# Kernel optimization log

Measured on AMD Instinct MI355X. Metric: run time of the kernel, lower is better.

The kernel has to match this reference:

```python
import jax, jax.numpy as jnp
import numpy as np

N, D_IN, D_OUT, E = 100000, 64, 64, 800000
C_IN, C_OUT = 1.0, 1.0
MAX_NORM = 1e6   # manifold.max_norm clamp used by PseudoHypAgg
EPS = 1e-15
BALL_EPS = 4e-3  # Poincare-ball projection margin (fp32)


def _artanh(x):
    return jnp.arctanh(jnp.clip(x, -1 + 1e-7, 1 - 1e-7))


def _proj(x, c):
    # project onto the open Poincare ball of curvature c
    sqrt_c = jnp.sqrt(c)
    norm = jnp.clip(jnp.linalg.norm(x, axis=-1, keepdims=True), EPS)
    maxn = (1.0 - BALL_EPS) / sqrt_c
    return jnp.where(norm > maxn, x / norm * maxn, x)


def _expmap0(u, c):
    sqrt_c = jnp.sqrt(c)
    n = jnp.clip(jnp.linalg.norm(u, axis=-1, keepdims=True), EPS)
    return jnp.tanh(sqrt_c * n) * u / (sqrt_c * n)


def _logmap0(p, c):
    sqrt_c = jnp.sqrt(c)
    n = jnp.clip(jnp.linalg.norm(p, axis=-1, keepdims=True), EPS)
    return _artanh(sqrt_c * n) * p / (sqrt_c * n)


def _mobius_add(x, y, c):
    x2 = jnp.sum(x * x, -1, keepdims=True)
    y2 = jnp.sum(y * y, -1, keepdims=True)
    xy = jnp.sum(x * y, -1, keepdims=True)
    num = (1 + 2 * c * xy + c * y2) * x + (1 - c * x2) * y
    den = 1 + 2 * c * xy + c * c * x2 * y2
    return num / jnp.clip(den, EPS)


def _mobius_matvec(M, x, c):
    sqrt_c = jnp.sqrt(c)
    x_norm = jnp.clip(jnp.linalg.norm(x, axis=-1, keepdims=True), EPS)
    mx = x @ M.T  # [N, D_OUT]
    mx_norm = jnp.clip(jnp.linalg.norm(mx, axis=-1, keepdims=True), EPS)
    res = jnp.tanh(mx_norm / x_norm * _artanh(sqrt_c * x_norm)) * mx / (mx_norm * sqrt_c)
    zero = jnp.all(mx == 0, axis=-1, keepdims=True)
    return jnp.where(zero, jnp.zeros_like(res), res)


def setup_inputs() -> dict:
    key = jax.random.key(0)
    k1, k2, k3, k4, k5, k6 = jax.random.split(key, 6)
    # node features: small-norm points inside the unit ball
    x = _proj(0.05 * jax.random.normal(k1, (N, D_IN), jnp.float32), C_IN)
    W = jax.random.normal(k2, (D_OUT, D_IN), jnp.float32) / np.float32(np.sqrt(D_IN))
    b = 0.01 * jax.random.normal(k3, (D_OUT,), jnp.float32)
    edge_row = jax.random.randint(k4, (E,), 0, N, jnp.int32)
    edge_col = jax.random.randint(k5, (E,), 0, N, jnp.int32)
    edge_val = jax.random.uniform(k6, (E,), jnp.float32) / 16.0  # ~normalized adj weights
    return {"x": x, "W": W, "b": b, "edge_row": edge_row,
            "edge_col": edge_col, "edge_val": edge_val}


def reference(x, W, b, edge_row, edge_col, edge_val):
    # --- PseudoHypLinear (eval mode: dropout inactive) ---
    mv = _mobius_matvec(W, x, C_IN)
    res = _proj(mv, C_IN)
    hyp_b = _proj(_expmap0(b[None, :], C_IN), C_IN)  # proj_tan0 is identity on the ball
    h = _proj(_mobius_add(res, hyp_b, C_IN), C_IN)
    # --- PseudoHypAgg (use_att=False): spmm in tangent space at origin ---
    x_t = _logmap0(h, C_IN)                              # [N, D_OUT]
    msg = edge_val[:, None] * x_t[edge_col]              # [E, D_OUT]
    support_t = jax.ops.segment_sum(msg, edge_row, num_segments=N)
    support_t = jnp.minimum(support_t, MAX_NORM)         # clamp(max=manifold.max_norm)
    h = _proj(_expmap0(support_t, C_IN), C_IN)           # proj_tan0 identity
    # --- PseudoHypAct: act in tangent at origin (c_in), re-embed with c_out ---
    xt = jax.nn.relu(_logmap0(h, C_IN))
    return _proj(_expmap0(xt, C_OUT), C_OUT)
```

## Files before the change

### kernel.cpp

```cpp
#include <hip/hip_runtime.h>
#include <hip/hip_fp16.h>
#include <math.h>

#define DD 64
#define BK 128
#define BCAP 2048
#define NBKT_MAX 800
#define CHUNK 8192
constexpr float FEPS = 1e-15f;
constexpr float MAXN = 1.0f - 4e-3f;

__device__ __forceinline__ float wsum(float v) {
    v += __shfl_xor(v, 32);
    v += __shfl_xor(v, 16);
    v += __shfl_xor(v, 8);
    v += __shfl_xor(v, 4);
    v += __shfl_xor(v, 2);
    v += __shfl_xor(v, 1);
    return v;
}

__device__ __forceinline__ int wave_incl_scan(int v) {
    int lane = threadIdx.x & 63;
    #pragma unroll
    for (int d = 1; d < 64; d <<= 1) {
        int t = __shfl_up(v, d);
        if (lane >= d) v += t;
    }
    return v;
}

__device__ __forceinline__ float artanh_c(float x) {
    x = fminf(fmaxf(x, -1.f + 1e-7f), 1.f - 1e-7f);
    return 0.5f * logf((1.f + x) / (1.f - x));
}

struct SmemLin {
    float tile[DD * 65];
    float red0[8][DD];
    float red1[8][DD];
    float hb[66];
};
struct SmemBin {
    int lcnt[NBKT_MAX];
    int goff[NBKT_MAX];
};

__global__ __launch_bounds__(512) void kfused(
    const float* __restrict__ x, const float* __restrict__ W,
    const float* __restrict__ bvec, __half* __restrict__ xth,
    const int* __restrict__ erow, const int* __restrict__ ecol,
    const float* __restrict__ eval_, int* __restrict__ gcnt,
    int2* __restrict__ binned, int nbkt, int n_edges, int n_nodes, int nbL) {
    __shared__ union { SmemLin lin; SmemBin bin; } sm;
    const int t = threadIdx.x;

    if ((int)blockIdx.x >= nbL) {
        const int eb = ((int)blockIdx.x - nbL) * CHUNK;
        for (int i = t; i < nbkt; i += 512) sm.bin.lcnt[i] = 0;
        __syncthreads();
        int rk[16];
        #pragma unroll
        for (int i = 0; i < 16; ++i) {
            int e = eb + i * 512 + t;
            rk[i] = -1;
            if (e < n_edges) {
                int r = erow[e];
                int bkt = r >> 7;
                int rank = atomicAdd(&sm.bin.lcnt[bkt], 1);
                rk[i] = (bkt << 20) | ((r & (BK - 1)) << 13) | rank;
            }
        }
        __syncthreads();
        for (int i = t; i < nbkt; i += 512) {
            int c = sm.bin.lcnt[i];
            if (c > 0) sm.bin.goff[i] = atomicAdd(&gcnt[i], c);
        }
        __syncthreads();
        #pragma unroll
        for (int i = 0; i < 16; ++i) {
            int e = eb + i * 512 + t;
            if (e >= n_edges) continue;
            int bkt = rk[i] >> 20, lr = (rk[i] >> 13) & 127, rank = rk[i] & 8191;
            int pos = sm.bin.goff[bkt] + rank;
            if (pos < BCAP)
                binned[(size_t)bkt * BCAP + pos] =
                    make_int2((lr << 17) | ecol[e], __float_as_int(eval_[e]));
        }
        return;
    }

    const int lane = t & 63;
    const int w = t >> 6;
    const int n0 = blockIdx.x * DD;

    #pragma unroll
    for (int rep = 0; rep < 2; ++rep) {
        int i = rep * 512 + t;
        int nd = i >> 4, q = i & 15;
        int node = n0 + nd;
        const float4* src = reinterpret_cast<const float4*>(
            x + (size_t)(node < n_nodes ? node : 0) * DD);
        float4 v = src[q];
        float* d = &sm.lin.tile[nd * 65 + q * 4];
        d[0] = v.x; d[1] = v.y; d[2] = v.z; d[3] = v.w;
    }
    if (t < 64) {
        float bv = bvec[t];
        float n2 = wsum(bv * bv);
        float n = fmaxf(sqrtf(n2), FEPS);
        float th = tanhf(n);
        float p = th * (bv / n);
        float pn = th * (sqrtf(n2) / n);
        float pn_c = fmaxf(pn, FEPS);
        if (pn_c > MAXN) p *= MAXN / pn_c;
        sm.lin.hb[t] = p;
        float p2 = wsum(p * p);
        if (t == 0) sm.lin.hb[DD] = p2;
    }
    __syncthreads();

    const int jbase = __builtin_amdgcn_readfirstlane(w) * 8;
    float mx[8] = {0.f, 0.f, 0.f, 0.f, 0.f, 0.f, 0.f, 0.f};
    float xn2 = 0.f;
    #pragma unroll
    for (int kk = 0; kk < 4; ++kk) {
        float xv[16];
        #pragma unroll
        for (int ki = 0; ki < 16; ++ki)
            xv[ki] = sm.lin.tile[lane * 65 + kk * 16 + ki];
        #pragma unroll
        for (int ki = 0; ki < 16; ++ki)
            xn2 = fmaf(xv[ki], xv[ki], xn2);
        #pragma unroll
        for (int jj = 0; jj < 8; ++jj) {
            const float* Wr = W + (jbase + jj) * DD + kk * 16;
            float a = mx[jj];
            #pragma unroll
            for (int ki = 0; ki < 16; ++ki) a = fmaf(Wr[ki], xv[ki], a);
            mx[jj] = a;
        }
    }
    float mx2p = 0.f, mxhp = 0.f;
    #pragma unroll
    for (int jj = 0; jj < 8; ++jj) {
        mx2p = fmaf(mx[jj], mx[jj], mx2p);
        mxhp = fmaf(mx[jj], sm.lin.hb[jbase + jj], mxhp);
    }
    sm.lin.red0[w][lane] = mx2p;
    sm.lin.red1[w][lane] = mxhp;
    __syncthreads();
    float mx2 = 0.f, mxh = 0.f;
    #pragma unroll
    for (int ww = 0; ww < 8; ++ww) {
        mx2 += sm.lin.red0[ww][lane];
        mxh += sm.lin.red1[ww][lane];
    }

    float xn = fmaxf(sqrtf(xn2), FEPS);
    float mxn = fmaxf(sqrtf(mx2), FEPS);
    float th = tanhf((mxn / xn) * artanh_c(xn));
    float sres = (mx2 == 0.f) ? 0.f : th / mxn;
    float rn = (mx2 == 0.f) ? 0.f : th * (sqrtf(mx2) / mxn);
    float rn_c = fmaxf(rn, FEPS);
    float s1 = (rn_c > MAXN) ? sres * (MAXN / rn_c) : sres;
    float x2r = s1 * s1 * mx2;
    float xy = s1 * mxh;
    float y2 = sm.lin.hb[DD];
    float ca = 1.f + 2.f * xy + y2;
    float cb = 1.f - x2r;
    float rden = 1.f / fmaxf(1.f + 2.f * xy + x2r * y2, FEPS);
    float al = ca * s1 * rden;
    float be = cb * rden;
    float h2 = al * al * mx2 + 2.f * al * be * mxh + be * be * y2;
    float hn = fmaxf(sqrtf(h2), FEPS);
    float sh = 1.f;
    if (hn > MAXN) { sh = MAXN / hn; hn = MAXN; }
    float su = sh * (artanh_c(hn) / hn);
    float A = su * al, B = su * be;

    #pragma unroll
    for (int jj = 0; jj < 8; ++jj)
        sm.lin.tile[lane * 65 + jbase + jj] =
            fmaf(A, mx[jj], B * sm.lin.hb[jbase + jj]);
    __syncthreads();

    uint2* dst = reinterpret_cast<uint2*>(xth + (size_t)n0 * DD);
    #pragma unroll
    for (int rep = 0; rep < 2; ++rep) {
        int i = rep * 512 + t;
        int nd = i >> 4, q = i & 15;
        if (n0 + nd < n_nodes) {
            const float* s = &sm.lin.tile[nd * 65 + q * 4];
            __half2 h0 = __floats2half2_rn(s[0], s[1]);
            __half2 h1 = __floats2half2_rn(s[2], s[3]);
            uint2 o;
            o.x = *reinterpret_cast<unsigned int*>(&h0);
            o.y = *reinterpret_cast<unsigned int*>(&h1);
            dst[i] = o;
        }
    }
}

__device__ __forceinline__ void agg_epilogue(
    float4 acc, int row, int fl, float* __restrict__ out) {
    float4 s;
    s.x = fminf(acc.x, 1e6f); s.y = fminf(acc.y, 1e6f);
    s.z = fminf(acc.z, 1e6f); s.w = fminf(acc.w, 1e6f);
    float4 rs;
    rs.x = fmaxf(s.x, 0.f); rs.y = fmaxf(s.y, 0.f);
    rs.z = fmaxf(s.z, 0.f); rs.w = fmaxf(s.w, 0.f);
    float n2p = s.x * s.x + s.y * s.y + s.z * s.z + s.w * s.w;
    float sp2p = rs.x * rs.x + rs.y * rs.y + rs.z * rs.z + rs.w * rs.w;
    #pragma unroll
    for (int m = 1; m < 16; m <<= 1) {
        n2p += __shfl_xor(n2p, m);
        sp2p += __shfl_xor(sp2p, m);
    }
    float n = fmaxf(sqrtf(n2p), FEPS);
    float th = tanhf(n);
    float c1 = th / n;
    float pn = th * (sqrtf(n2p) / n);
    float pn_c = fmaxf(pn, FEPS);
    if (pn_c > MAXN) { c1 *= MAXN / pn_c; pn_c = MAXN; }
    float k1 = (artanh_c(pn_c) / pn_c) * c1;
    float u2 = k1 * k1 * sp2p;
    float un = fmaxf(sqrtf(u2), FEPS);
    float t2 = tanhf(un);
    float k2 = (t2 / un) * k1;
    float on = t2 * (sqrtf(u2) / un);
    float on_c = fmaxf(on, FEPS);
    if (on_c > MAXN) k2 *= MAXN / on_c;
    float4 o;
    o.x = k2 * rs.x; o.y = k2 * rs.y; o.z = k2 * rs.z; o.w = k2 * rs.w;
    reinterpret_cast<float4*>(out)[(size_t)row * 16 + fl] = o;
}

__global__ __launch_bounds__(512) void kagg2(
    const int* __restrict__ gcnt, const int2* __restrict__ binned,
    const __half* __restrict__ xth, float* __restrict__ out, int n_nodes) {
    __shared__ int hist[BK], offs[BK], cur[BK];
    __shared__ int2 srt[BCAP];
    const int t = threadIdx.x;
    const int b = blockIdx.x;
    for (int i = t; i < BK; i += 512) hist[i] = 0;
    __syncthreads();
    const int nrec = min(gcnt[b], BCAP);
    const int2* rec = binned + (size_t)b * BCAP;
    int2 rc[BCAP / 512];
    #pragma unroll
    for (int i = 0; i < BCAP / 512; ++i) {
        int j = i * 512 + t;
        if (j < nrec) {
            rc[i] = rec[j];
            atomicAdd(&hist[rc[i].x >> 17], 1);
        }
    }
    __syncthreads();
    if (t < 64) {
        int v = hist[t];
        int s = wave_incl_scan(v);
        offs[t] = s - v;
    }
    __syncthreads();
    if (t < 64) {
        int c = offs[63] + hist[63];
        int v = hist[64 + t];
        int s = wave_incl_scan(v);
        offs[64 + t] = c + s - v;
    }
    __syncthreads();
    for (int i = t; i < BK; i += 512) cur[i] = offs[i];
    __syncthreads();
    #pragma unroll
    for (int i = 0; i < BCAP / 512; ++i) {
        int j = i * 512 + t;
        if (j < nrec) {
            int lr = rc[i].x >> 17;
            int p = atomicAdd(&cur[lr], 1);
            srt[p] = make_int2(rc[i].x & 0x1FFFF, rc[i].y);
        }
    }
    __syncthreads();

    const int g = t >> 4, fl = t & 15;
    #pragma unroll
    for (int it = 0; it < BK / 32; ++it) {
        int lr = it * 32 + g;
        int row = b * BK + lr;
        if (row >= n_nodes) continue;
        int beg = offs[lr], end = beg + hist[lr];
        float4 acc = make_float4(0.f, 0.f, 0.f, 0.f);
        int j = beg;
        for (; j + 3 < end; j += 4) {
            int2 e0 = srt[j], e1 = srt[j + 1], e2 = srt[j + 2], e3 = srt[j + 3];
            float2 r0 = *reinterpret_cast<const float2*>(xth + (size_t)e0.x * DD + fl * 4);
            float2 r1 = *reinterpret_cast<const float2*>(xth + (size_t)e1.x * DD + fl * 4);
            float2 r2 = *reinterpret_cast<const float2*>(xth + (size_t)e2.x * DD + fl * 4);
            float2 r3 = *reinterpret_cast<const float2*>(xth + (size_t)e3.x * DD + fl * 4);
            float w0 = __int_as_float(e0.y), w1 = __int_as_float(e1.y);
            float w2 = __int_as_float(e2.y), w3 = __int_as_float(e3.y);
            float2 a0 = __half22float2(*reinterpret_cast<__half2*>(&r0.x));
            float2 a1 = __half22float2(*reinterpret_cast<__half2*>(&r0.y));
            float2 b0 = __half22float2(*reinterpret_cast<__half2*>(&r1.x));
            float2 b1 = __half22float2(*reinterpret_cast<__half2*>(&r1.y));
            float2 c0 = __half22float2(*reinterpret_cast<__half2*>(&r2.x));
            float2 c1 = __half22float2(*reinterpret_cast<__half2*>(&r2.y));
            float2 d0 = __half22float2(*reinterpret_cast<__half2*>(&r3.x));
            float2 d1 = __half22float2(*reinterpret_cast<__half2*>(&r3.y));
            acc.x = fmaf(w0, a0.x, acc.x); acc.y = fmaf(w0, a0.y, acc.y);
            acc.z = fmaf(w0, a1.x, acc.z); acc.w = fmaf(w0, a1.y, acc.w);
            acc.x = fmaf(w1, b0.x, acc.x); acc.y = fmaf(w1, b0.y, acc.y);
            acc.z = fmaf(w1, b1.x, acc.z); acc.w = fmaf(w1, b1.y, acc.w);
            acc.x = fmaf(w2, c0.x, acc.x); acc.y = fmaf(w2, c0.y, acc.y);
            acc.z = fmaf(w2, c1.x, acc.z); acc.w = fmaf(w2, c1.y, acc.w);
            acc.x = fmaf(w3, d0.x, acc.x); acc.y = fmaf(w3, d0.y, acc.y);
            acc.z = fmaf(w3, d1.x, acc.z); acc.w = fmaf(w3, d1.y, acc.w);
        }
        for (; j < end; ++j) {
            int2 e = srt[j];
            float2 r0 = *reinterpret_cast<const float2*>(xth + (size_t)e.x * DD + fl * 4);
            float w0 = __int_as_float(e.y);
            float2 a0 = __half22float2(*reinterpret_cast<__half2*>(&r0.x));
            float2 a1 = __half22float2(*reinterpret_cast<__half2*>(&r0.y));
            acc.x = fmaf(w0, a0.x, acc.x); acc.y = fmaf(w0, a0.y, acc.y);
            acc.z = fmaf(w0, a1.x, acc.z); acc.w = fmaf(w0, a1.y, acc.w);
        }
        agg_epilogue(acc, row, fl, out);
    }
}

extern "C" void kernel_launch(void* const* d_in, const int* in_sizes, int n_in,
                              void* d_out, int out_size, void* d_ws, size_t ws_size,
                              hipStream_t stream) {
    const float* x     = (const float*)d_in[0];
    const float* W     = (const float*)d_in[1];
    const float* b     = (const float*)d_in[2];
    const int*   erow  = (const int*)d_in[3];
    const int*   ecol  = (const int*)d_in[4];
    const float* eval_ = (const float*)d_in[5];
    const int n_nodes = in_sizes[0] / DD;
    const int n_edges = in_sizes[3];
    float* out = (float*)d_out;

    const int NBKT = (n_nodes + BK - 1) / BK;

    int2*   binned = (int2*)d_ws;
    __half* xth    = (__half*)(binned + (size_t)NBKT * BCAP);
    int*    gcnt   = (int*)(xth + (size_t)n_nodes * DD);

    const int nbB = (n_edges + CHUNK - 1) / CHUNK;
    const int nbL = (n_nodes + DD - 1) / DD;

    hipMemsetAsync(gcnt, 0, NBKT_MAX * sizeof(int), stream);
    kfused<<<nbL + nbB, 512, 0, stream>>>(x, W, b, xth, erow, ecol, eval_,
                                          gcnt, binned, NBKT, n_edges, n_nodes, nbL);
    kagg2<<<NBKT, 512, 0, stream>>>(gcnt, binned, xth, out, n_nodes);
}
```

Measured before the change: 148.8 us.

## Shrink binning chunks, schedule binning blocks first, and streamline linear epilogue

The edge-binning chunk shrinks from 8192 to 2048 edges per block, giving more and lighter binning blocks, and those blocks now occupy the low block indices so they are dispatched before the linear-transform blocks. The linear epilogue now has only the first wave compute the per-node scale factors into shared memory. Each thread then writes its 8 half values directly with one 16-byte store, instead of staging through the shared tile and doing a second transposed pass. Smaller chunks raise the number of global atomics on bucket counters and repeat the per-block clearing of the bucket-count array.

```diff
diff --git a/kernel.cpp b/kernel.cpp
--- a/kernel.cpp
+++ b/kernel.cpp
@@ -6,7 +6,7 @@
 #define BK 128
 #define BCAP 2048
 #define NBKT_MAX 800
-#define CHUNK 8192
+#define CHUNK 2048
 constexpr float FEPS = 1e-15f;
 constexpr float MAXN = 1.0f - 4e-3f;
 
@@ -40,6 +40,7 @@
     float red0[8][DD];
     float red1[8][DD];
     float hb[66];
+    float Ab[DD], Bb[DD];
 };
 struct SmemBin {
     int lcnt[NBKT_MAX];
@@ -51,17 +52,17 @@
     const float* __restrict__ bvec, __half* __restrict__ xth,
     const int* __restrict__ erow, const int* __restrict__ ecol,
     const float* __restrict__ eval_, int* __restrict__ gcnt,
-    int2* __restrict__ binned, int nbkt, int n_edges, int n_nodes, int nbL) {
+    int2* __restrict__ binned, int nbkt, int n_edges, int n_nodes, int nbB) {
     __shared__ union { SmemLin lin; SmemBin bin; } sm;
     const int t = threadIdx.x;
 
-    if ((int)blockIdx.x >= nbL) {
-        const int eb = ((int)blockIdx.x - nbL) * CHUNK;
+    if ((int)blockIdx.x < nbB) {
+        const int eb = blockIdx.x * CHUNK;
         for (int i = t; i < nbkt; i += 512) sm.bin.lcnt[i] = 0;
         __syncthreads();
-        int rk[16];
-        #pragma unroll
-        for (int i = 0; i < 16; ++i) {
+        int rk[4];
+        #pragma unroll
+        for (int i = 0; i < 4; ++i) {
             int e = eb + i * 512 + t;
             rk[i] = -1;
             if (e < n_edges) {
@@ -78,7 +79,7 @@
         }
         __syncthreads();
         #pragma unroll
-        for (int i = 0; i < 16; ++i) {
+        for (int i = 0; i < 4; ++i) {
             int e = eb + i * 512 + t;
             if (e >= n_edges) continue;
             int bkt = rk[i] >> 20, lr = (rk[i] >> 13) & 127, rank = rk[i] & 8191;
@@ -92,7 +93,7 @@
 
     const int lane = t & 63;
     const int w = t >> 6;
-    const int n0 = blockIdx.x * DD;
+    const int n0 = ((int)blockIdx.x - nbB) * DD;
 
     #pragma unroll
     for (int rep = 0; rep < 2; ++rep) {
@@ -150,55 +151,56 @@
     sm.lin.red0[w][lane] = mx2p;
     sm.lin.red1[w][lane] = mxhp;
     __syncthreads();
-    float mx2 = 0.f, mxh = 0.f;
-    #pragma unroll
-    for (int ww = 0; ww < 8; ++ww) {
-        mx2 += sm.lin.red0[ww][lane];
-        mxh += sm.lin.red1[ww][lane];
-    }
-
-    float xn = fmaxf(sqrtf(xn2), FEPS);
-    float mxn = fmaxf(sqrtf(mx2), FEPS);
-    float th = tanhf((mxn / xn) * artanh_c(xn));
-    float sres = (mx2 == 0.f) ? 0.f : th / mxn;
-    float rn = (mx2 == 0.f) ? 0.f : th * (sqrtf(mx2) / mxn);
-    float rn_c = fmaxf(rn, FEPS);
-    float s1 = (rn_c > MAXN) ? sres * (MAXN / rn_c) : sres;
-    float x2r = s1 * s1 * mx2;
-    float xy = s1 * mxh;
-    float y2 = sm.lin.hb[DD];
-    float ca = 1.f + 2.f * xy + y2;
-    float cb = 1.f - x2r;
-    float rden = 1.f / fmaxf(1.f + 2.f * xy + x2r * y2, FEPS);
-    float al = ca * s1 * rden;
-    float be = cb * rden;
-    float h2 = al * al * mx2 + 2.f * al * be * mxh + be * be * y2;
-    float hn = fmaxf(sqrtf(h2), FEPS);
-    float sh = 1.f;
-    if (hn > MAXN) { sh = MAXN / hn; hn = MAXN; }
-    float su = sh * (artanh_c(hn) / hn);
-    float A = su * al, B = su * be;
-
-    #pragma unroll
-    for (int jj = 0; jj < 8; ++jj)
-        sm.lin.tile[lane * 65 + jbase + jj] =
-            fmaf(A, mx[jj], B * sm.lin.hb[jbase + jj]);
-    __syncthreads();
-
-    uint2* dst = reinterpret_cast<uint2*>(xth + (size_t)n0 * DD);
-    #pragma unroll
-    for (int rep = 0; rep < 2; ++rep) {
-        int i = rep * 512 + t;
-        int nd = i >> 4, q = i & 15;
-        if (n0 + nd < n_nodes) {
-            const float* s = &sm.lin.tile[nd * 65 + q * 4];
-            __half2 h0 = __floats2half2_rn(s[0], s[1]);
-            __half2 h1 = __floats2half2_rn(s[2], s[3]);
-            uint2 o;
-            o.x = *reinterpret_cast<unsigned int*>(&h0);
-            o.y = *reinterpret_cast<unsigned int*>(&h1);
-            dst[i] = o;
-        }
+
+    if (t < 64) {
+        float mx2 = 0.f, mxh = 0.f;
+        #pragma unroll
+        for (int ww = 0; ww < 8; ++ww) {
+            mx2 += sm.lin.red0[ww][t];
+            mxh += sm.lin.red1[ww][t];
+        }
+        float xn = fmaxf(sqrtf(xn2), FEPS);
+        float mxn = fmaxf(sqrtf(mx2), FEPS);
+        float th = tanhf((mxn / xn) * artanh_c(xn));
+        float sres = (mx2 == 0.f) ? 0.f : th / mxn;
+        float rn = (mx2 == 0.f) ? 0.f : th * (sqrtf(mx2) / mxn);
+        float rn_c = fmaxf(rn, FEPS);
+        float s1 = (rn_c > MAXN) ? sres * (MAXN / rn_c) : sres;
+        float x2r = s1 * s1 * mx2;
+        float xy = s1 * mxh;
+        float y2 = sm.lin.hb[DD];
+        float ca = 1.f + 2.f * xy + y2;
+        float cb = 1.f - x2r;
+        float rden = 1.f / fmaxf(1.f + 2.f * xy + x2r * y2, FEPS);
+        float al = ca * s1 * rden;
+        float be = cb * rden;
+        float h2 = al * al * mx2 + 2.f * al * be * mxh + be * be * y2;
+        float hn = fmaxf(sqrtf(h2), FEPS);
+        float sh = 1.f;
+        if (hn > MAXN) { sh = MAXN / hn; hn = MAXN; }
+        float su = sh * (artanh_c(hn) / hn);
+        sm.lin.Ab[t] = su * al;
+        sm.lin.Bb[t] = su * be;
+    }
+    __syncthreads();
+
+    int node = n0 + lane;
+    if (node < n_nodes) {
+        float A = sm.lin.Ab[lane], B = sm.lin.Bb[lane];
+        float u[8];
+        #pragma unroll
+        for (int jj = 0; jj < 8; ++jj)
+            u[jj] = fmaf(A, mx[jj], B * sm.lin.hb[jbase + jj]);
+        __half2 p0 = __floats2half2_rn(u[0], u[1]);
+        __half2 p1 = __floats2half2_rn(u[2], u[3]);
+        __half2 p2 = __floats2half2_rn(u[4], u[5]);
+        __half2 p3 = __floats2half2_rn(u[6], u[7]);
+        uint4 o;
+        o.x = *reinterpret_cast<unsigned int*>(&p0);
+        o.y = *reinterpret_cast<unsigned int*>(&p1);
+        o.z = *reinterpret_cast<unsigned int*>(&p2);
+        o.w = *reinterpret_cast<unsigned int*>(&p3);
+        *reinterpret_cast<uint4*>(xth + (size_t)node * DD + jbase) = o;
     }
 }
 
@@ -353,7 +355,7 @@
     const int nbL = (n_nodes + DD - 1) / DD;
 
     hipMemsetAsync(gcnt, 0, NBKT_MAX * sizeof(int), stream);
-    kfused<<<nbL + nbB, 512, 0, stream>>>(x, W, b, xth, erow, ecol, eval_,
-                                          gcnt, binned, NBKT, n_edges, n_nodes, nbL);
+    kfused<<<nbB + nbL, 512, 0, stream>>>(x, W, b, xth, erow, ecol, eval_,
+                                          gcnt, binned, NBKT, n_edges, n_nodes, nbB);
     kagg2<<<NBKT, 512, 0, stream>>>(gcnt, binned, xth, out, n_nodes);
 }
```

Result: faster. 138.9 us (-6.7%).
